# Performance work log

Hardware: AMD Instinct MI355X
Metric: run time of the kernel (lower is better)

Reference implementation:

```python
import jax, jax.numpy as jnp
import numpy as np

N, E, D, ED, G = 100000, 1600000, 64, 64, 512  # nodes, edges, node_dim, edge_dim, graphs
LN_EPS = 1e-5


def setup_inputs() -> dict:
    key = jax.random.key(0)
    ks = jax.random.split(key, 16)
    s_e = 1.0 / np.sqrt(ED)
    s_n = 1.0 / np.sqrt(D)
    inp = {
        'x': jax.random.normal(ks[0], (N, D), jnp.float32),
        'edge_index': jax.random.randint(ks[1], (2, E), 0, N, dtype=jnp.int32),
        'edge_attr': jax.random.normal(ks[2], (E, ED), jnp.float32),
        'node2graph': jnp.sort(jax.random.randint(ks[3], (N,), 0, G, dtype=jnp.int32)),
        # conv1 params
        'We1': jax.random.normal(ks[4], (ED, D), jnp.float32) * s_e,
        'be1': jnp.zeros((D,), jnp.float32),
        'Wm1': jax.random.normal(ks[5], (D, D), jnp.float32) * s_n,
        'bm1': jnp.zeros((D,), jnp.float32),
        'eps1': jnp.array([0.1], jnp.float32),
        'gamma1': jnp.ones((D,), jnp.float32),
        'beta1': jnp.zeros((D,), jnp.float32),
        # conv2 params
        'We2': jax.random.normal(ks[6], (ED, D), jnp.float32) * s_e,
        'be2': jnp.zeros((D,), jnp.float32),
        'Wm2': jax.random.normal(ks[7], (D, D), jnp.float32) * s_n,
        'bm2': jnp.zeros((D,), jnp.float32),
        'eps2': jnp.array([0.1], jnp.float32),
        'gamma2': jnp.ones((D,), jnp.float32),
        'beta2': jnp.zeros((D,), jnp.float32),
    }
    return inp


def _gine_conv(x, src, dst, edge_attr, We, be, Wm, bm, eps):
    # message: SiLU(Wm @ relu(x_j + SiLU(We @ e)) )  gathered per edge, scatter-added to dst
    ea = jax.nn.silu(edge_attr @ We + be)                     # (E, D)
    msg = jax.nn.silu(jnp.maximum(x[src] + ea, 0.0) @ Wm + bm)  # (E, D)
    agg = jax.ops.segment_sum(msg, dst, num_segments=x.shape[0])
    return agg + (1.0 + eps) * x


def _graph_norm(x, g, gamma, beta):
    # pyg LayerNorm(mode='graph'): normalize over all nodes*channels per graph
    f = x.shape[1]
    cnt = jax.ops.segment_sum(jnp.ones((x.shape[0],), x.dtype), g, num_segments=G) * f
    cnt = jnp.maximum(cnt, 1.0)
    mean = jax.ops.segment_sum(x.sum(-1), g, num_segments=G) / cnt          # (G,)
    var = jax.ops.segment_sum((x * x).sum(-1), g, num_segments=G) / cnt - mean ** 2
    xn = (x - mean[g][:, None]) / jnp.sqrt(var + LN_EPS)[g][:, None]
    return xn * gamma + beta


def reference(x, edge_index, edge_attr, node2graph,
              We1, be1, Wm1, bm1, eps1, gamma1, beta1,
              We2, be2, Wm2, bm2, eps2, gamma2, beta2):
    src, dst = edge_index[0], edge_index[1]
    identity = x
    # branch 1 (NOTE: the original torch code computes conv1->norm->relu but then
    # overwrites `out` with conv2(x, ...); we reproduce that faithfully)
    out = _gine_conv(x, src, dst, edge_attr, We1, be1, Wm1, bm1, eps1)
    out = _graph_norm(out, node2graph, gamma1, beta1)
    out = jnp.maximum(out, 0.0)
    # branch 2 (takes original x, per source)
    out = _gine_conv(x, src, dst, edge_attr, We2, be2, Wm2, bm2, eps2)
    out = _graph_norm(out, node2graph, gamma2, beta2)
    out = out + identity
    return jnp.maximum(out, 0.0)
```

## Files before the change

### kernel.cpp

```cpp
#include <hip/hip_runtime.h>
#include <math.h>

#define NN 100000
#define NE 1600000
#define NG 512
#define LN_EPS 1e-5f

typedef __attribute__((ext_vector_type(8))) short short8;
typedef __attribute__((ext_vector_type(4))) float floatx4;

union BF8U { short8 v; unsigned u[4]; };
union F4   { floatx4 v; float f[4]; };

static __device__ __forceinline__ unsigned pk_bf2(float a, float b) {
    union { float f; unsigned u; } A, B;
    A.f = a; B.f = b;
    const unsigned ua = A.u + 0x8000u;
    const unsigned ub = B.u + 0x8000u;
    return __builtin_amdgcn_perm(ub, ua, 0x07060302u);
}
static __device__ __forceinline__ float silu_f(float v) {
    return v * __builtin_amdgcn_rcpf(1.0f + __expf(-v));
}

__global__ __launch_bounds__(256)
void xconv_kernel(const float* __restrict__ x, unsigned* __restrict__ x_bf)
{
    const int total = NN * 32;
    for (int i = blockIdx.x * blockDim.x + threadIdx.x; i < total;
         i += gridDim.x * blockDim.x) {
        const float2 v = *(const float2*)(x + (size_t)i * 2);
        x_bf[i] = pk_bf2(v.x, v.y);
    }
}

__global__ __launch_bounds__(256)
void hist_kernel(const int* __restrict__ dst, int* __restrict__ cnt)
{
    for (int e = blockIdx.x * blockDim.x + threadIdx.x; e < NE;
         e += gridDim.x * blockDim.x)
        atomicAdd(&cnt[dst[e]], 1);
}

#define SCAN_CHUNK 1024
#define SCAN_NB ((NN + SCAN_CHUNK - 1) / SCAN_CHUNK)

__global__ __launch_bounds__(256)
void scan_partial_kernel(const int* __restrict__ cnt, int* __restrict__ bsums)
{
    __shared__ int sdata[256];
    const int b = blockIdx.x, t = threadIdx.x;
    const int base = b * SCAN_CHUNK + t * 4;
    int s = 0;
    #pragma unroll
    for (int i = 0; i < 4; ++i) {
        const int idx = base + i;
        s += (idx < NN) ? cnt[idx] : 0;
    }
    sdata[t] = s;
    __syncthreads();
    for (int off = 128; off > 0; off >>= 1) {
        if (t < off) sdata[t] += sdata[t + off];
        __syncthreads();
    }
    if (t == 0) bsums[b] = sdata[0];
}

__global__ __launch_bounds__(128)
void scan_top_kernel(int* __restrict__ bsums)
{
    __shared__ int s[128];
    const int t = threadIdx.x;
    const int v = (t < SCAN_NB) ? bsums[t] : 0;
    s[t] = v;
    __syncthreads();
    for (int off = 1; off < 128; off <<= 1) {
        const int u = (t >= off) ? s[t - off] : 0;
        __syncthreads();
        s[t] += u;
        __syncthreads();
    }
    if (t < SCAN_NB) bsums[t] = s[t] - v;
}

__global__ __launch_bounds__(256)
void scan_final_kernel(int* __restrict__ cnt, const int* __restrict__ bsums)
{
    __shared__ int sdata[256];
    const int b = blockIdx.x, t = threadIdx.x;
    const int base = b * SCAN_CHUNK + t * 4;
    int c[4];
    #pragma unroll
    for (int i = 0; i < 4; ++i) {
        const int idx = base + i;
        c[i] = (idx < NN) ? cnt[idx] : 0;
    }
    const int tsum = c[0] + c[1] + c[2] + c[3];
    sdata[t] = tsum;
    __syncthreads();
    for (int off = 1; off < 256; off <<= 1) {
        const int v = (t >= off) ? sdata[t - off] : 0;
        __syncthreads();
        sdata[t] += v;
        __syncthreads();
    }
    int off0 = bsums[b] + sdata[t] - tsum;
    #pragma unroll
    for (int i = 0; i < 4; ++i) {
        const int idx = base + i;
        if (idx < NN) cnt[idx] = off0;
        off0 += c[i];
    }
}

__global__ __launch_bounds__(256)
void scatter_kernel(const int* __restrict__ src, const int* __restrict__ dst,
                    int* __restrict__ starts,
                    int2* __restrict__ ps, int* __restrict__ dsts_s)
{
    for (int e = blockIdx.x * blockDim.x + threadIdx.x; e < NE;
         e += gridDim.x * blockDim.x) {
        const int d = dst[e];
        const int pos = atomicAdd(&starts[d], 1);
        ps[pos] = make_int2(e, src[e]);
        dsts_s[pos] = d;
    }
}

#define EK_BLOCKS 2048
#define EK_WAVES (EK_BLOCKS * 4)

__global__ __launch_bounds__(256)
void edge_kernel_sorted(const unsigned* __restrict__ x_bf,
                        const int2* __restrict__ ps,
                        const int* __restrict__ dsts_s,
                        const float* __restrict__ eattr,
                        const float* __restrict__ We,
                        const float* __restrict__ be,
                        const float* __restrict__ Wm,
                        const float* __restrict__ bm,
                        float* __restrict__ agg)
{
    __shared__ float ltile[4][16 * 68];
    const int lane = threadIdx.x & 63;
    const int wid  = threadIdx.x >> 6;
    const int m = lane & 15;
    const int q = lane >> 4;
    float* tile = ltile[wid];

    short8 wef[2][4], wmf[2][4];
    float bev[4], bmv[4];
    #pragma unroll
    for (int kh = 0; kh < 2; ++kh)
        #pragma unroll
        for (int t = 0; t < 4; ++t) {
            BF8U fe, fm;
            #pragma unroll
            for (int p = 0; p < 4; ++p) {
                const int k = kh * 32 + q * 8 + p * 2;
                const int n = m + 16 * t;
                fe.u[p] = pk_bf2(We[k * 64 + n], We[(k + 1) * 64 + n]);
                fm.u[p] = pk_bf2(Wm[k * 64 + n], Wm[(k + 1) * 64 + n]);
            }
            wef[kh][t] = fe.v; wmf[kh][t] = fm.v;
        }
    #pragma unroll
    for (int t = 0; t < 4; ++t) { bev[t] = be[m + 16 * t]; bmv[t] = bm[m + 16 * t]; }

    const int n_tiles = NE / 16;
    const int tpw = (n_tiles + EK_WAVES - 1) / EK_WAVES;
    const int w = blockIdx.x * 4 + wid;
    const int tl0 = w * tpw;
    const int tl1 = min(n_tiles, tl0 + tpw);
    if (tl0 >= tl1) return;

    int2 pv = ps[tl0 * 16 + m];
    int4 dnv = *(const int4*)&dsts_s[tl0 * 16 + q * 4];
    floatx4 ea[4];
    {
        const float* p = eattr + (size_t)pv.x * 64 + q * 8;
        ea[0] = *(const floatx4*)p;        ea[1] = *(const floatx4*)(p + 4);
        ea[2] = *(const floatx4*)(p + 32); ea[3] = *(const floatx4*)(p + 36);
    }

    float cv[4] = {0.f, 0.f, 0.f, 0.f};
    int cd = -1;

    for (int tl = tl0; tl < tl1; ++tl) {
        const bool haveNext = (tl + 1 < tl1);
        int2 pvn = pv; int4 dnn = dnv; floatx4 ean[4];
        if (haveNext) {
            const int e0n = (tl + 1) * 16;
            pvn = ps[e0n + m];
            dnn = *(const int4*)&dsts_s[e0n + q * 4];
            const float* p = eattr + (size_t)pvn.x * 64 + q * 8;
            ean[0] = *(const floatx4*)p;        ean[1] = *(const floatx4*)(p + 4);
            ean[2] = *(const floatx4*)(p + 32); ean[3] = *(const floatx4*)(p + 36);
        }
        const uint4 xa = *(const uint4*)(x_bf + (size_t)pv.y * 32 + q * 4);
        const uint4 xb = *(const uint4*)(x_bf + (size_t)pv.y * 32 + 16 + q * 4);

        short8 a1[2];
        {
            F4 u0, u1, u2, u3;
            u0.v = ea[0]; u1.v = ea[1]; u2.v = ea[2]; u3.v = ea[3];
            BF8U f0, f1;
            f0.u[0] = pk_bf2(u0.f[0], u0.f[1]);
            f0.u[1] = pk_bf2(u0.f[2], u0.f[3]);
            f0.u[2] = pk_bf2(u1.f[0], u1.f[1]);
            f0.u[3] = pk_bf2(u1.f[2], u1.f[3]);
            f1.u[0] = pk_bf2(u2.f[0], u2.f[1]);
            f1.u[1] = pk_bf2(u2.f[2], u2.f[3]);
            f1.u[2] = pk_bf2(u3.f[0], u3.f[1]);
            f1.u[3] = pk_bf2(u3.f[2], u3.f[3]);
            a1[0] = f0.v; a1[1] = f1.v;
        }
        floatx4 acc[4];
        #pragma unroll
        for (int t = 0; t < 4; ++t) acc[t] = (floatx4){0.f, 0.f, 0.f, 0.f};
        #pragma unroll
        for (int kh = 0; kh < 2; ++kh)
            #pragma unroll
            for (int t = 0; t < 4; ++t)
                acc[t] = __builtin_amdgcn_mfma_f32_16x16x32_bf16(a1[kh], wef[kh][t], acc[t], 0, 0, 0);

        #pragma unroll
        for (int t = 0; t < 4; ++t)
            #pragma unroll
            for (int r = 0; r < 4; ++r)
                tile[(q * 4 + r) * 68 + m + 16 * t] = silu_f(acc[t][r] + bev[t]);
        __asm__ volatile("s_waitcnt lgkmcnt(0)" ::: "memory");

        short8 a2[2];
        {
            const float* lp = &tile[m * 68 + q * 8];
            F4 A0, A1, B0, B1;
            A0.v = *(const floatx4*)lp;        A1.v = *(const floatx4*)(lp + 4);
            B0.v = *(const floatx4*)(lp + 32); B1.v = *(const floatx4*)(lp + 36);
            const unsigned xu[8] = {xa.x, xa.y, xa.z, xa.w, xb.x, xb.y, xb.z, xb.w};
            float el[16];
            el[0]=A0.f[0]; el[1]=A0.f[1]; el[2]=A0.f[2]; el[3]=A0.f[3];
            el[4]=A1.f[0]; el[5]=A1.f[1]; el[6]=A1.f[2]; el[7]=A1.f[3];
            el[8]=B0.f[0]; el[9]=B0.f[1]; el[10]=B0.f[2]; el[11]=B0.f[3];
            el[12]=B1.f[0]; el[13]=B1.f[1]; el[14]=B1.f[2]; el[15]=B1.f[3];
            BF8U f0, f1;
            #pragma unroll
            for (int p = 0; p < 8; ++p) {
                union { unsigned u; float f; } lo, hi;
                lo.u = xu[p] << 16; hi.u = xu[p] & 0xffff0000u;
                const float t0 = fmaxf(lo.f + el[p * 2],     0.0f);
                const float t1 = fmaxf(hi.f + el[p * 2 + 1], 0.0f);
                const unsigned pk = pk_bf2(t0, t1);
                if (p < 4) f0.u[p] = pk; else f1.u[p - 4] = pk;
            }
            a2[0] = f0.v; a2[1] = f1.v;
        }
        #pragma unroll
        for (int t = 0; t < 4; ++t) acc[t] = (floatx4){0.f, 0.f, 0.f, 0.f};
        #pragma unroll
        for (int kh = 0; kh < 2; ++kh)
            #pragma unroll
            for (int t = 0; t < 4; ++t)
                acc[t] = __builtin_amdgcn_mfma_f32_16x16x32_bf16(a2[kh], wmf[kh][t], acc[t], 0, 0, 0);

        float sv[4][4];
        #pragma unroll
        for (int t = 0; t < 4; ++t)
            #pragma unroll
            for (int r = 0; r < 4; ++r)
                sv[t][r] = silu_f(acc[t][r] + bmv[t]);

        const int dn[4] = {dnv.x, dnv.y, dnv.z, dnv.w};
        #define FLUSH(DN, VAL)                                                  \
            do {                                                                \
                atomicAdd(agg + (size_t)(DN) * 64 + m,      (VAL)[0]);          \
                atomicAdd(agg + (size_t)(DN) * 64 + m + 16, (VAL)[1]);          \
                atomicAdd(agg + (size_t)(DN) * 64 + m + 32, (VAL)[2]);          \
                atomicAdd(agg + (size_t)(DN) * 64 + m + 48, (VAL)[3]);          \
            } while (0)

        float run[4], head[4] = {0.f, 0.f, 0.f, 0.f};
        const int hd = dn[0];
        int rd = dn[0];
        bool headClosed = false;
        #pragma unroll
        for (int t = 0; t < 4; ++t) run[t] = sv[t][0];
        #pragma unroll
        for (int r = 1; r < 4; ++r) {
            if (dn[r] == rd) {
                #pragma unroll
                for (int t = 0; t < 4; ++t) run[t] += sv[t][r];
            } else {
                if (!headClosed) {
                    #pragma unroll
                    for (int t = 0; t < 4; ++t) head[t] = run[t];
                    headClosed = true;
                } else {
                    FLUSH(rd, run);
                }
                #pragma unroll
                for (int t = 0; t < 4; ++t) run[t] = sv[t][r];
                rd = dn[r];
            }
        }
        const bool pure = !headClosed;
        float tail[4]; const int td = rd;
        #pragma unroll
        for (int t = 0; t < 4; ++t) tail[t] = run[t];

        float tl_[4]; int td_;
        #pragma unroll
        for (int t = 0; t < 4; ++t) tl_[t] = tail[t];
        td_ = td;
        #pragma unroll
        for (int g = 0; g < 4; ++g) {
            float iv[4]; int ivd;
            if (g == 0) {
                #pragma unroll
                for (int t = 0; t < 4; ++t) iv[t] = cv[t];
                ivd = cd;
            } else {
                const int sl = m + (g - 1) * 16;
                #pragma unroll
                for (int t = 0; t < 4; ++t) iv[t] = __shfl(tl_[t], sl, 64);
                ivd = __shfl(td_, (g - 1) * 16, 64);
            }
            const int hdg = __shfl(hd, g * 16, 64);
            const bool mine = (q == g);
            if (ivd == hdg) {
                if (mine) {
                    if (pure) {
                        #pragma unroll
                        for (int t = 0; t < 4; ++t) tl_[t] += iv[t];
                    } else {
                        #pragma unroll
                        for (int t = 0; t < 4; ++t) head[t] += iv[t];
                    }
                }
            } else {
                if (g == 0) {
                    if (q == 0 && cd >= 0) FLUSH(cd, iv);
                } else {
                    if (q == g - 1) FLUSH(td_, tl_);
                }
            }
            if (mine && !pure) FLUSH(hd, head);
        }
        #pragma unroll
        for (int t = 0; t < 4; ++t) cv[t] = __shfl(tl_[t], m + 48, 64);
        cd = __shfl(td_, 48, 64);

        pv = pvn; dnv = dnn;
        #pragma unroll
        for (int t = 0; t < 4; ++t) ea[t] = ean[t];
    }
    if (q == 0 && cd >= 0) {
        atomicAdd(agg + (size_t)cd * 64 + m,      cv[0]);
        atomicAdd(agg + (size_t)cd * 64 + m + 16, cv[1]);
        atomicAdd(agg + (size_t)cd * 64 + m + 32, cv[2]);
        atomicAdd(agg + (size_t)cd * 64 + m + 48, cv[3]);
    }
    #undef FLUSH
}

__global__ __launch_bounds__(256)
void edge_kernel_unsorted(const float* __restrict__ x,
                          const int* __restrict__ src,
                          const int* __restrict__ dst,
                          const float* __restrict__ eattr,
                          const float* __restrict__ We,
                          const float* __restrict__ be,
                          const float* __restrict__ Wm,
                          const float* __restrict__ bm,
                          float* __restrict__ agg)
{
    __shared__ float ltile[4][16 * 68];
    const int lane = threadIdx.x & 63;
    const int wid  = threadIdx.x >> 6;
    const int m = lane & 15;
    const int q = lane >> 4;
    float* tile = ltile[wid];

    short8 wef[2][4], wmf[2][4];
    float bev[4], bmv[4];
    #pragma unroll
    for (int kh = 0; kh < 2; ++kh)
        #pragma unroll
        for (int t = 0; t < 4; ++t) {
            BF8U fe, fm;
            #pragma unroll
            for (int p = 0; p < 4; ++p) {
                const int k = kh * 32 + q * 8 + p * 2;
                const int n = m + 16 * t;
                fe.u[p] = pk_bf2(We[k * 64 + n], We[(k + 1) * 64 + n]);
                fm.u[p] = pk_bf2(Wm[k * 64 + n], Wm[(k + 1) * 64 + n]);
            }
            wef[kh][t] = fe.v; wmf[kh][t] = fm.v;
        }
    #pragma unroll
    for (int t = 0; t < 4; ++t) { bev[t] = be[m + 16 * t]; bmv[t] = bm[m + 16 * t]; }

    const int n_tiles = NE / 16;
    const int stride = gridDim.x * 4;
    for (int tl = blockIdx.x * 4 + wid; tl < n_tiles; tl += stride) {
        const int e0 = tl * 16;
        short8 a1[2];
        #pragma unroll
        for (int kh = 0; kh < 2; ++kh) {
            const float* p = eattr + (size_t)(e0 + m) * 64 + kh * 32 + q * 8;
            F4 v0, v1; v0.v = *(const floatx4*)p; v1.v = *(const floatx4*)(p + 4);
            BF8U f;
            f.u[0] = pk_bf2(v0.f[0], v0.f[1]);
            f.u[1] = pk_bf2(v0.f[2], v0.f[3]);
            f.u[2] = pk_bf2(v1.f[0], v1.f[1]);
            f.u[3] = pk_bf2(v1.f[2], v1.f[3]);
            a1[kh] = f.v;
        }
        floatx4 acc[4];
        #pragma unroll
        for (int t = 0; t < 4; ++t) acc[t] = (floatx4){0.f, 0.f, 0.f, 0.f};
        #pragma unroll
        for (int kh = 0; kh < 2; ++kh)
            #pragma unroll
            for (int t = 0; t < 4; ++t)
                acc[t] = __builtin_amdgcn_mfma_f32_16x16x32_bf16(a1[kh], wef[kh][t], acc[t], 0, 0, 0);
        #pragma unroll
        for (int t = 0; t < 4; ++t)
            #pragma unroll
            for (int r = 0; r < 4; ++r)
                tile[(q * 4 + r) * 68 + m + 16 * t] = silu_f(acc[t][r] + bev[t]);
        __asm__ volatile("s_waitcnt lgkmcnt(0)" ::: "memory");
        const int sn = src[e0 + m];
        short8 a2[2];
        {
            const float* lp = &tile[m * 68 + q * 8];
            const float* xp = x + (size_t)sn * 64 + q * 8;
            F4 a, b, c, d, X0, X1, X2, X3;
            a.v = *(const floatx4*)lp;        b.v = *(const floatx4*)(lp + 4);
            c.v = *(const floatx4*)(lp + 32); d.v = *(const floatx4*)(lp + 36);
            X0.v = *(const floatx4*)xp;        X1.v = *(const floatx4*)(xp + 4);
            X2.v = *(const floatx4*)(xp + 32); X3.v = *(const floatx4*)(xp + 36);
            BF8U f0, f1;
            f0.u[0] = pk_bf2(fmaxf(a.f[0]+X0.f[0],0.f), fmaxf(a.f[1]+X0.f[1],0.f));
            f0.u[1] = pk_bf2(fmaxf(a.f[2]+X0.f[2],0.f), fmaxf(a.f[3]+X0.f[3],0.f));
            f0.u[2] = pk_bf2(fmaxf(b.f[0]+X1.f[0],0.f), fmaxf(b.f[1]+X1.f[1],0.f));
            f0.u[3] = pk_bf2(fmaxf(b.f[2]+X1.f[2],0.f), fmaxf(b.f[3]+X1.f[3],0.f));
            f1.u[0] = pk_bf2(fmaxf(c.f[0]+X2.f[0],0.f), fmaxf(c.f[1]+X2.f[1],0.f));
            f1.u[1] = pk_bf2(fmaxf(c.f[2]+X2.f[2],0.f), fmaxf(c.f[3]+X2.f[3],0.f));
            f1.u[2] = pk_bf2(fmaxf(d.f[0]+X3.f[0],0.f), fmaxf(d.f[1]+X3.f[1],0.f));
            f1.u[3] = pk_bf2(fmaxf(d.f[2]+X3.f[2],0.f), fmaxf(d.f[3]+X3.f[3],0.f));
            a2[0] = f0.v; a2[1] = f1.v;
        }
        #pragma unroll
        for (int t = 0; t < 4; ++t) acc[t] = (floatx4){0.f, 0.f, 0.f, 0.f};
        #pragma unroll
        for (int kh = 0; kh < 2; ++kh)
            #pragma unroll
            for (int t = 0; t < 4; ++t)
                acc[t] = __builtin_amdgcn_mfma_f32_16x16x32_bf16(a2[kh], wmf[kh][t], acc[t], 0, 0, 0);
        int dn[4];
        #pragma unroll
        for (int r = 0; r < 4; ++r) dn[r] = dst[e0 + q * 4 + r];
        #pragma unroll
        for (int t = 0; t < 4; ++t)
            #pragma unroll
            for (int r = 0; r < 4; ++r)
                atomicAdd(agg + (size_t)dn[r] * 64 + m + 16 * t, silu_f(acc[t][r] + bmv[t]));
    }
}

#define STATS_WAVES 4096
__global__ __launch_bounds__(256)
void stats_kernel(const float* __restrict__ agg,
                  const float* __restrict__ x,
                  const int* __restrict__ n2g,
                  const float* __restrict__ eps,
                  float* __restrict__ gsum,
                  float* __restrict__ gss,
                  float* __restrict__ gcnt)
{
    const int lane = threadIdx.x & 63;
    const int wid  = threadIdx.x >> 6;
    const int w    = blockIdx.x * 4 + wid;
    const int chunk = (NN + STATS_WAVES - 1) / STATS_WAVES;
    const int n0 = w * chunk;
    const int n1 = min(NN, n0 + chunk);
    if (n0 >= n1) return;
    const float k = 1.0f + eps[0];

    int   curg = n2g[n0];
    float s = 0.f, ss = 0.f, rc = 0.f;
    for (int n = n0; n < n1; ++n) {
        const int g = n2g[n];
        if (g != curg) {
            float a = s, b = ss;
            #pragma unroll
            for (int off = 32; off > 0; off >>= 1) {
                a += __shfl_down(a, off, 64);
                b += __shfl_down(b, off, 64);
            }
            if (lane == 0) {
                atomicAdd(&gsum[curg], a);
                atomicAdd(&gss[curg], b);
                atomicAdd(&gcnt[curg], rc);
            }
            s = 0.f; ss = 0.f; rc = 0.f; curg = g;
        }
        const float pre = agg[(size_t)n * 64 + lane] + k * x[(size_t)n * 64 + lane];
        s += pre; ss += pre * pre; rc += (lane == 0) ? 1.0f : 0.0f;
    }
    float a = s, b = ss;
    #pragma unroll
    for (int off = 32; off > 0; off >>= 1) {
        a += __shfl_down(a, off, 64);
        b += __shfl_down(b, off, 64);
    }
    if (lane == 0) {
        atomicAdd(&gsum[curg], a);
        atomicAdd(&gss[curg], b);
        atomicAdd(&gcnt[curg], rc);
    }
}

__global__ __launch_bounds__(256)
void norm_kernel(const float* __restrict__ x,
                 const int* __restrict__ n2g,
                 const float* __restrict__ eps,
                 const float* __restrict__ gamma,
                 const float* __restrict__ beta,
                 const float* __restrict__ gsum,
                 const float* __restrict__ gss,
                 const float* __restrict__ gcnt,
                 float* __restrict__ out)
{
    const float k = 1.0f + eps[0];
    const int total = NN * 16;
    for (int idx = blockIdx.x * blockDim.x + threadIdx.x; idx < total;
         idx += gridDim.x * blockDim.x) {
        const int n  = idx >> 4;
        const int c4 = (idx & 15) * 4;
        const int g  = n2g[n];
        const float cnt  = fmaxf(gcnt[g] * 64.0f, 1.0f);
        const float mean = gsum[g] / cnt;
        const float var  = gss[g] / cnt - mean * mean;
        const float rsig = rsqrtf(var + LN_EPS);
        F4 a, xv, o;
        a.v  = *(const floatx4*)&out[(size_t)n * 64 + c4];
        xv.v = *(const floatx4*)&x[(size_t)n * 64 + c4];
        #pragma unroll
        for (int j = 0; j < 4; ++j) {
            const float pre = a.f[j] + k * xv.f[j];
            const float v = (pre - mean) * rsig * gamma[c4 + j] + beta[c4 + j] + xv.f[j];
            o.f[j] = fmaxf(v, 0.0f);
        }
        *(floatx4*)&out[(size_t)n * 64 + c4] = o.v;
    }
}

extern "C" void kernel_launch(void* const* d_in, const int* in_sizes, int n_in,
                              void* d_out, int out_size, void* d_ws, size_t ws_size,
                              hipStream_t stream)
{
    const float* x      = (const float*)d_in[0];
    const int*   ei     = (const int*)  d_in[1];
    const float* eattr  = (const float*)d_in[2];
    const int*   n2g    = (const int*)  d_in[3];
    const float* We2    = (const float*)d_in[11];
    const float* be2    = (const float*)d_in[12];
    const float* Wm2    = (const float*)d_in[13];
    const float* bm2    = (const float*)d_in[14];
    const float* eps2   = (const float*)d_in[15];
    const float* gamma2 = (const float*)d_in[16];
    const float* beta2  = (const float*)d_in[17];
    const int* src = ei;
    const int* dst = ei + NE;

    float* out  = (float*)d_out;
    float* gsum = (float*)d_ws;
    float* gss  = gsum + NG;
    float* gcnt = gss + NG;
    int*  bsums  = (int*)(gcnt + NG);
    int*  cnt    = bsums + 128;
    int*  dsts_s = cnt + NN;
    int2* ps     = (int2*)(dsts_s + NE);
    unsigned* x_bf = (unsigned*)(ps + NE);
    const size_t ws_need = (size_t)(3 * NG + 128 + NN + NE + 2 * (size_t)NE
                                    + (size_t)NN * 32) * 4;
    const bool do_sort = ws_size >= ws_need;

    hipMemsetAsync(d_out, 0, (size_t)NN * 64 * sizeof(float), stream);
    if (do_sort) {
        hipMemsetAsync(d_ws, 0, (size_t)(3 * NG + 128 + NN) * 4, stream);
        xconv_kernel<<<dim3(512), dim3(256), 0, stream>>>(x, x_bf);
        hist_kernel<<<dim3(512), dim3(256), 0, stream>>>(dst, cnt);
        scan_partial_kernel<<<dim3(SCAN_NB), dim3(256), 0, stream>>>(cnt, bsums);
        scan_top_kernel<<<dim3(1), dim3(128), 0, stream>>>(bsums);
        scan_final_kernel<<<dim3(SCAN_NB), dim3(256), 0, stream>>>(cnt, bsums);
        scatter_kernel<<<dim3(512), dim3(256), 0, stream>>>(src, dst, cnt, ps, dsts_s);
        edge_kernel_sorted<<<dim3(EK_BLOCKS), dim3(256), 0, stream>>>(
            x_bf, ps, dsts_s, eattr, We2, be2, Wm2, bm2, out);
    } else {
        hipMemsetAsync(d_ws, 0, 3 * NG * sizeof(float), stream);
        edge_kernel_unsorted<<<dim3(2048), dim3(256), 0, stream>>>(
            x, src, dst, eattr, We2, be2, Wm2, bm2, out);
    }
    stats_kernel<<<dim3(STATS_WAVES / 4), dim3(256), 0, stream>>>(
        out, x, n2g, eps2, gsum, gss, gcnt);
    norm_kernel<<<dim3(1024), dim3(256), 0, stream>>>(
        x, n2g, eps2, gamma2, beta2, gsum, gss, gcnt, out);
}
```

Measured before the change: 883.7 us.

## Deepen edge-kernel index prefetch to two tiles and fuse xconv with histogram

The sorted edge kernel now fetches permutation and destination indices two tiles ahead, so the edge-attribute gather for the next tile no longer waits on an index load issued in the same iteration. This is meant to hide the dependent-load latency of the index-then-gather chain. The x-to-bf16 conversion and the destination histogram are merged into one launch with a larger grid, saving a kernel launch. The deeper prefetch keeps more registers live, which may reduce occupancy.

```diff
diff --git a/kernel.cpp b/kernel.cpp
--- a/kernel.cpp
+++ b/kernel.cpp
@@ -24,21 +24,17 @@
 }
 
 __global__ __launch_bounds__(256)
-void xconv_kernel(const float* __restrict__ x, unsigned* __restrict__ x_bf)
-{
-    const int total = NN * 32;
-    for (int i = blockIdx.x * blockDim.x + threadIdx.x; i < total;
-         i += gridDim.x * blockDim.x) {
+void prep_kernel(const float* __restrict__ x, unsigned* __restrict__ x_bf,
+                 const int* __restrict__ dst, int* __restrict__ cnt)
+{
+    const int gsz = gridDim.x * blockDim.x;
+    const int tid = blockIdx.x * blockDim.x + threadIdx.x;
+    const int totx = NN * 32;
+    for (int i = tid; i < totx; i += gsz) {
         const float2 v = *(const float2*)(x + (size_t)i * 2);
         x_bf[i] = pk_bf2(v.x, v.y);
     }
-}
-
-__global__ __launch_bounds__(256)
-void hist_kernel(const int* __restrict__ dst, int* __restrict__ cnt)
-{
-    for (int e = blockIdx.x * blockDim.x + threadIdx.x; e < NE;
-         e += gridDim.x * blockDim.x)
+    for (int e = tid; e < NE; e += gsz)
         atomicAdd(&cnt[dst[e]], 1);
 }
 
@@ -174,11 +170,14 @@
     const int tl1 = min(n_tiles, tl0 + tpw);
     if (tl0 >= tl1) return;
 
-    int2 pv = ps[tl0 * 16 + m];
-    int4 dnv = *(const int4*)&dsts_s[tl0 * 16 + q * 4];
+    int2 pvA = ps[tl0 * 16 + m];
+    int4 dnA = *(const int4*)&dsts_s[tl0 * 16 + q * 4];
+    const int tB0 = min(tl0 + 1, tl1 - 1);
+    int2 pvB = ps[tB0 * 16 + m];
+    int4 dnB = *(const int4*)&dsts_s[tB0 * 16 + q * 4];
     floatx4 ea[4];
     {
-        const float* p = eattr + (size_t)pv.x * 64 + q * 8;
+        const float* p = eattr + (size_t)pvA.x * 64 + q * 8;
         ea[0] = *(const floatx4*)p;        ea[1] = *(const floatx4*)(p + 4);
         ea[2] = *(const floatx4*)(p + 32); ea[3] = *(const floatx4*)(p + 36);
     }
@@ -187,18 +186,17 @@
     int cd = -1;
 
     for (int tl = tl0; tl < tl1; ++tl) {
-        const bool haveNext = (tl + 1 < tl1);
-        int2 pvn = pv; int4 dnn = dnv; floatx4 ean[4];
-        if (haveNext) {
-            const int e0n = (tl + 1) * 16;
-            pvn = ps[e0n + m];
-            dnn = *(const int4*)&dsts_s[e0n + q * 4];
-            const float* p = eattr + (size_t)pvn.x * 64 + q * 8;
+        const int tC = min(tl + 2, tl1 - 1);
+        const int2 pvC = ps[tC * 16 + m];
+        const int4 dnC = *(const int4*)&dsts_s[tC * 16 + q * 4];
+        floatx4 ean[4];
+        {
+            const float* p = eattr + (size_t)pvB.x * 64 + q * 8;
             ean[0] = *(const floatx4*)p;        ean[1] = *(const floatx4*)(p + 4);
             ean[2] = *(const floatx4*)(p + 32); ean[3] = *(const floatx4*)(p + 36);
         }
-        const uint4 xa = *(const uint4*)(x_bf + (size_t)pv.y * 32 + q * 4);
-        const uint4 xb = *(const uint4*)(x_bf + (size_t)pv.y * 32 + 16 + q * 4);
+        const uint4 xa = *(const uint4*)(x_bf + (size_t)pvA.y * 32 + q * 4);
+        const uint4 xb = *(const uint4*)(x_bf + (size_t)pvA.y * 32 + 16 + q * 4);
 
         short8 a1[2];
         {
@@ -263,14 +261,13 @@
             for (int t = 0; t < 4; ++t)
                 acc[t] = __builtin_amdgcn_mfma_f32_16x16x32_bf16(a2[kh], wmf[kh][t], acc[t], 0, 0, 0);
 
-        float sv[4][4];
         #pragma unroll
         for (int t = 0; t < 4; ++t)
             #pragma unroll
             for (int r = 0; r < 4; ++r)
-                sv[t][r] = silu_f(acc[t][r] + bmv[t]);
-
-        const int dn[4] = {dnv.x, dnv.y, dnv.z, dnv.w};
+                acc[t][r] = silu_f(acc[t][r] + bmv[t]);
+
+        const int dn[4] = {dnA.x, dnA.y, dnA.z, dnA.w};
         #define FLUSH(DN, VAL)                                                  \
             do {                                                                \
                 atomicAdd(agg + (size_t)(DN) * 64 + m,      (VAL)[0]);          \
@@ -284,12 +281,12 @@
         int rd = dn[0];
         bool headClosed = false;
         #pragma unroll
-        for (int t = 0; t < 4; ++t) run[t] = sv[t][0];
+        for (int t = 0; t < 4; ++t) run[t] = acc[t][0];
         #pragma unroll
         for (int r = 1; r < 4; ++r) {
             if (dn[r] == rd) {
                 #pragma unroll
-                for (int t = 0; t < 4; ++t) run[t] += sv[t][r];
+                for (int t = 0; t < 4; ++t) run[t] += acc[t][r];
             } else {
                 if (!headClosed) {
                     #pragma unroll
@@ -299,19 +296,16 @@
                     FLUSH(rd, run);
                 }
                 #pragma unroll
-                for (int t = 0; t < 4; ++t) run[t] = sv[t][r];
+                for (int t = 0; t < 4; ++t) run[t] = acc[t][r];
                 rd = dn[r];
             }
         }
         const bool pure = !headClosed;
-        float tail[4]; const int td = rd;
-        #pragma unroll
-        for (int t = 0; t < 4; ++t) tail[t] = run[t];
-
         float tl_[4]; int td_;
         #pragma unroll
-        for (int t = 0; t < 4; ++t) tl_[t] = tail[t];
-        td_ = td;
+        for (int t = 0; t < 4; ++t) tl_[t] = run[t];
+        td_ = rd;
+
         #pragma unroll
         for (int g = 0; g < 4; ++g) {
             float iv[4]; int ivd;
@@ -350,7 +344,8 @@
         for (int t = 0; t < 4; ++t) cv[t] = __shfl(tl_[t], m + 48, 64);
         cd = __shfl(td_, 48, 64);
 
-        pv = pvn; dnv = dnn;
+        pvA = pvB; dnA = dnB;
+        pvB = pvC; dnB = dnC;
         #pragma unroll
         for (int t = 0; t < 4; ++t) ea[t] = ean[t];
     }
@@ -591,8 +586,7 @@
     hipMemsetAsync(d_out, 0, (size_t)NN * 64 * sizeof(float), stream);
     if (do_sort) {
         hipMemsetAsync(d_ws, 0, (size_t)(3 * NG + 128 + NN) * 4, stream);
-        xconv_kernel<<<dim3(512), dim3(256), 0, stream>>>(x, x_bf);
-        hist_kernel<<<dim3(512), dim3(256), 0, stream>>>(dst, cnt);
+        prep_kernel<<<dim3(768), dim3(256), 0, stream>>>(x, x_bf, dst, cnt);
         scan_partial_kernel<<<dim3(SCAN_NB), dim3(256), 0, stream>>>(cnt, bsums);
         scan_top_kernel<<<dim3(1), dim3(128), 0, stream>>>(bsums);
         scan_final_kernel<<<dim3(SCAN_NB), dim3(256), 0, stream>>>(cnt, bsums);
```

New measurement: 899.1 us. No clear change (+1.7%).
